# Kernel optimization log

Hardware: AMD Instinct MI355X
Metric: run time of the kernel (lower is better)

The kernel has to match this reference:

```python
import jax, jax.numpy as jnp
import numpy as np

E, D, A, F, K = 512, 1024, 128, 32, 31  # encoder_dim, decoder_dim, attention_dim, location_filters, kernel
B, T = 128, 512


def setup_inputs() -> dict:
    key = jax.random.key(0)
    ks = jax.random.split(key, 9)
    s = lambda *sh: 1.0 / np.sqrt(sh[-1])
    return {
        "encoder_outputs": jax.random.normal(ks[0], (B, T, E), jnp.float32),
        "decoder_state": jax.random.normal(ks[1], (B, D), jnp.float32),
        "prev_attention_weights": jax.random.uniform(ks[2], (B, T), jnp.float32),
        # parameters (torch Linear stores [out, in]; Conv1d [out, in, K])
        "W_enc": jax.random.normal(ks[3], (A, E), jnp.float32) * s(A, E),
        "W_dec": jax.random.normal(ks[4], (A, D), jnp.float32) * s(A, D),
        "conv_w": jax.random.normal(ks[5], (F, 1, K), jnp.float32) * (1.0 / np.sqrt(K)),
        "W_loc": jax.random.normal(ks[6], (A, F), jnp.float32) * s(A, F),
        "W_e": jax.random.normal(ks[7], (1, A), jnp.float32) * s(1, A),
        "b_e": jax.random.normal(ks[8], (1,), jnp.float32) * 0.01,
    }


def reference(encoder_outputs, decoder_state, prev_attention_weights,
              W_enc, W_dec, conv_w, W_loc, W_e, b_e):
    # encoder projection: [B,T,E] @ [E,A] -> [B,T,A]
    enc_p = jnp.einsum('bte,ae->bta', encoder_outputs, W_enc)
    # decoder projection: [B,D] -> [B,1,A]
    dec_p = jnp.einsum('bd,ad->ba', decoder_state, W_dec)[:, None, :]
    # location conv: [B,1,T] * [F,1,K] -> [B,F,T], 'same' padding
    loc = jax.lax.conv_general_dilated(
        prev_attention_weights[:, None, :], conv_w,
        window_strides=(1,), padding=[((K - 1) // 2, (K - 1) // 2)],
        dimension_numbers=('NCH', 'OIH', 'NCH'))
    # [B,F,T] -> [B,T,A]
    loc_p = jnp.einsum('bft,af->bta', loc, W_loc)
    # energies: [B,T]
    energies = jnp.einsum('bta,a->bt', jnp.tanh(enc_p + dec_p + loc_p), W_e[0]) + b_e[0]
    attention_weights = jax.nn.softmax(energies, axis=1)
    # context: [B,T] x [B,T,E] -> [B,E]
    context_vector = jnp.einsum('bt,bte->be', attention_weights, encoder_outputs)
    return context_vector, attention_weights
```

## Files before the change

### kernel.cpp

```cpp
#include <hip/hip_runtime.h>
#include <hip/hip_bf16.h>
#include <math.h>

namespace {
constexpr int EDIM  = 512;
constexpr int DDIM  = 1024;
constexpr int ADIM  = 128;
constexpr int FDIM  = 32;
constexpr int KW    = 31;
constexpr int BATCH = 128;
constexpr int TDIM  = 512;

typedef __attribute__((ext_vector_type(8))) short short8;
typedef __attribute__((ext_vector_type(4))) float floatx4;

__device__ __forceinline__ float fast_tanh(float x) {
  x = fminf(9.0f, fmaxf(-9.0f, x));
  float e = __expf(2.0f * x);
  return (e - 1.0f) / (e + 1.0f);
}

__device__ __forceinline__ ushort2 pack_bf16(float x, float y) {
  union { __hip_bfloat162 h; ushort2 u; } cv;
  cv.h = __float22bfloat162_rn(make_float2(x, y));
  return cv.u;
}

__device__ __forceinline__ short8 pack8(floatx4 a, floatx4 b) {
  union { ushort2 u[4]; short8 v; } o;
  o.u[0] = pack_bf16(a[0], a[1]); o.u[1] = pack_bf16(a[2], a[3]);
  o.u[2] = pack_bf16(b[0], b[1]); o.u[3] = pack_bf16(b[2], b[3]);
  return o.v;
}

__global__ __launch_bounds__(256)
void dec_proj_kernel(const float* __restrict__ dec,
                     const float* __restrict__ Wdec,
                     float* __restrict__ dec_p) {
  int b = blockIdx.x, az = blockIdx.y;
  int tid = threadIdx.x;
  int al = tid >> 3, seg = tid & 7;
  int a = az * 32 + al;
  const float* dv = dec + (size_t)b * DDIM;
  const float* wv = Wdec + (size_t)a * DDIM;
  float s = 0.f;
  #pragma unroll 8
  for (int it = 0; it < 32; ++it) {
    int d = it * 32 + seg * 4;
    float4 d4 = *(const float4*)(dv + d);
    float4 w4 = *(const float4*)(wv + d);
    s += d4.x * w4.x + d4.y * w4.y + d4.z * w4.z + d4.w * w4.w;
  }
  s += __shfl_xor(s, 1, 64);
  s += __shfl_xor(s, 2, 64);
  s += __shfl_xor(s, 4, 64);
  if (seg == 0) dec_p[b * ADIM + a] = s;
}

__global__ __launch_bounds__(256)
void energies_kernel(const float* __restrict__ enc,
                     const float* __restrict__ Wenc,
                     const float* __restrict__ pa,
                     const float* __restrict__ convw,
                     const float* __restrict__ Wloc,
                     const float* __restrict__ We,
                     const float* __restrict__ be,
                     const float* __restrict__ dec_p,
                     float* __restrict__ energ) {
  __shared__ ushort WencS[16384];
  __shared__ ushort convS[2048];
  __shared__ float pa_s[96];
  __shared__ float cw_s[FDIM * 33];

  const int tid  = threadIdx.x;
  const int b    = blockIdx.y;
  const int t0b  = blockIdx.x * 64;
  const int wave = tid >> 6, lane = tid & 63;
  const int lc = lane & 15, lq = lane >> 4;
  const int sw = lc & 7;

  if (tid < 94) {
    int gt = t0b - 15 + tid;
    pa_s[tid] = (gt >= 0 && gt < TDIM) ? pa[b * TDIM + gt] : 0.f;
  }
  for (int id = tid; id < FDIM * KW; id += 256)
    cw_s[(id / KW) * 33 + (id % KW)] = convw[id];
  __syncthreads();

  {
    const int tl = tid >> 2, fg = tid & 3;
    float cv[8];
    #pragma unroll
    for (int n = 0; n < 8; ++n) {
      int f = fg * 8 + n;
      float s = 0.f;
      #pragma unroll
      for (int k = 0; k < KW; ++k) s += pa_s[tl + k] * cw_s[f * 33 + k];
      cv[n] = s;
    }
    *(short8*)&convS[tl * 32 + fg * 8] =
        pack8((floatx4){cv[0], cv[1], cv[2], cv[3]},
              (floatx4){cv[4], cv[5], cv[6], cv[7]});
  }

  #pragma unroll
  for (int r = 0; r < 8; ++r) {
    int idx = tid + r * 256;
    int sup = idx >> 10, i2 = idx & 1023;
    int row = i2 >> 3, gc = (i2 & 7) ^ (row & 7);
    const float* g = Wenc + (size_t)row * EDIM + sup * 64 + gc * 8;
    *(short8*)&WencS[sup * 8192 + i2 * 8] =
        pack8(*(const floatx4*)g, *(const floatx4*)(g + 4));
  }

  const float* pA = enc + ((size_t)(b * TDIM + t0b + wave * 16 + lc)) * EDIM + lq * 8;
  floatx4 ca = *(const floatx4*)pA, cb = *(const floatx4*)(pA + 4);

  float dpv[8], wev[8];
  #pragma unroll
  for (int aT = 0; aT < 8; ++aT) {
    int a = aT * 16 + lc;
    dpv[aT] = dec_p[b * ADIM + a];
    wev[aT] = We[a];
  }

  floatx4 acc[8];
  #pragma unroll
  for (int aT = 0; aT < 8; ++aT) acc[aT] = (floatx4){0.f, 0.f, 0.f, 0.f};

  __syncthreads();

  for (int ph = 0; ph < 4; ++ph) {
    if (ph) {
      __syncthreads();
      #pragma unroll
      for (int r = 0; r < 8; ++r) {
        int idx = tid + r * 256;
        int sup = idx >> 10, i2 = idx & 1023;
        int row = i2 >> 3, gc = (i2 & 7) ^ (row & 7);
        const float* g = Wenc + (size_t)row * EDIM + ph * 128 + sup * 64 + gc * 8;
        *(short8*)&WencS[sup * 8192 + i2 * 8] =
            pack8(*(const floatx4*)g, *(const floatx4*)(g + 4));
      }
      __syncthreads();
    }
    #pragma unroll
    for (int st = 0; st < 4; ++st) {
      const int step = ph * 4 + st;
      floatx4 na = {0,0,0,0}, nb = {0,0,0,0};
      if (step < 15) {
        const float* q = pA + (step + 1) * 32;
        na = *(const floatx4*)q; nb = *(const floatx4*)(q + 4);
      }
      short8 af = pack8(ca, cb);
      const int cco = (((st & 1) * 4 + lq) ^ sw) * 8;
      const ushort* Bb = &WencS[(st >> 1) * 8192 + cco];
      #pragma unroll
      for (int aT = 0; aT < 8; ++aT) {
        short8 bf = *(const short8*)&Bb[(aT * 16 + lc) * 64];
        acc[aT] = __builtin_amdgcn_mfma_f32_16x16x32_bf16(af, bf, acc[aT], 0, 0, 0);
      }
      ca = na; cb = nb;
    }
  }

  {
    short8 afl = *(const short8*)&convS[(wave * 16 + lc) * 32 + lq * 8];
    #pragma unroll
    for (int aT = 0; aT < 8; ++aT) {
      const float* g = Wloc + (size_t)(aT * 16 + lc) * FDIM + lq * 8;
      short8 bfl = pack8(*(const floatx4*)g, *(const floatx4*)(g + 4));
      acc[aT] = __builtin_amdgcn_mfma_f32_16x16x32_bf16(afl, bfl, acc[aT], 0, 0, 0);
    }
  }

  const float be0 = be[0];
  {
    float es[4] = {0.f, 0.f, 0.f, 0.f};
    #pragma unroll
    for (int aT = 0; aT < 8; ++aT)
      #pragma unroll
      for (int i = 0; i < 4; ++i)
        es[i] += fast_tanh(acc[aT][i] + dpv[aT]) * wev[aT];
    #pragma unroll
    for (int m = 1; m < 16; m <<= 1)
      #pragma unroll
      for (int i = 0; i < 4; ++i) es[i] += __shfl_xor(es[i], m, 64);
    if (lc == 0) {
      floatx4 ev = {es[0] + be0, es[1] + be0, es[2] + be0, es[3] + be0};
      *(floatx4*)&energ[(size_t)b * TDIM + t0b + wave * 16 + lq * 4] = ev;
    }
  }
}

__global__ __launch_bounds__(256)
void softmax_context_kernel(const float* __restrict__ enc,
                            const float* __restrict__ energ,
                            float* __restrict__ attn,
                            float* __restrict__ ctx) {
  __shared__ float aw[TDIM];
  __shared__ float redm[4];
  __shared__ float reds[4];
  __shared__ float red2[128];
  const int b = blockIdx.y, ex = blockIdx.x, tid = threadIdx.x;
  const float* row = energ + (size_t)b * TDIM;
  float x0 = row[tid], x1 = row[tid + 256];
  float m = fmaxf(x0, x1);
  #pragma unroll
  for (int off = 32; off; off >>= 1) m = fmaxf(m, __shfl_xor(m, off, 64));
  int wid = tid >> 6, lane = tid & 63;
  if (lane == 0) redm[wid] = m;
  __syncthreads();
  m = fmaxf(fmaxf(redm[0], redm[1]), fmaxf(redm[2], redm[3]));
  float e0 = __expf(x0 - m), e1 = __expf(x1 - m);
  float s = e0 + e1;
  #pragma unroll
  for (int off = 32; off; off >>= 1) s += __shfl_xor(s, off, 64);
  if (lane == 0) reds[wid] = s;
  __syncthreads();
  s = reds[0] + reds[1] + reds[2] + reds[3];
  float inv = 1.0f / s;
  float w0 = e0 * inv, w1 = e1 * inv;
  aw[tid] = w0; aw[tid + 256] = w1;
  if (ex == 0) {
    attn[(size_t)b * TDIM + tid] = w0;
    attn[(size_t)b * TDIM + tid + 256] = w1;
  }
  __syncthreads();
  const int j = tid & 127, h = tid >> 7;
  const float* ep = enc + ((size_t)(b * TDIM + h * 256)) * EDIM + ex * 128 + j;
  float acc = 0.f;
  #pragma unroll 16
  for (int t = 0; t < 256; ++t) acc += aw[h * 256 + t] * ep[(size_t)t * EDIM];
  if (h == 1) red2[j] = acc;
  __syncthreads();
  if (h == 0) ctx[(size_t)b * EDIM + ex * 128 + j] = acc + red2[j];
}

__global__ __launch_bounds__(256)
void softmax_context_inplace_kernel(const float* __restrict__ enc,
                                    float* __restrict__ attn,
                                    float* __restrict__ ctx) {
  __shared__ float aw[TDIM];
  __shared__ float redm[4];
  __shared__ float reds[4];
  const int b = blockIdx.y, tid = threadIdx.x;
  float* row = attn + (size_t)b * TDIM;
  float x0 = row[tid], x1 = row[tid + 256];
  float m = fmaxf(x0, x1);
  #pragma unroll
  for (int off = 32; off; off >>= 1) m = fmaxf(m, __shfl_xor(m, off, 64));
  int wid = tid >> 6, lane = tid & 63;
  if (lane == 0) redm[wid] = m;
  __syncthreads();
  m = fmaxf(fmaxf(redm[0], redm[1]), fmaxf(redm[2], redm[3]));
  float e0 = __expf(x0 - m), e1 = __expf(x1 - m);
  float s = e0 + e1;
  #pragma unroll
  for (int off = 32; off; off >>= 1) s += __shfl_xor(s, off, 64);
  if (lane == 0) reds[wid] = s;
  __syncthreads();
  s = reds[0] + reds[1] + reds[2] + reds[3];
  float inv = 1.0f / s;
  float w0 = e0 * inv, w1 = e1 * inv;
  row[tid] = w0; row[tid + 256] = w1;
  aw[tid] = w0; aw[tid + 256] = w1;
  __syncthreads();
  const float* ep = enc + ((size_t)b * TDIM) * EDIM;
  float a0 = 0.f, a1 = 0.f;
  #pragma unroll 8
  for (int t = 0; t < TDIM; ++t) {
    float w = aw[t];
    a0 += w * ep[(size_t)t * EDIM + tid];
    a1 += w * ep[(size_t)t * EDIM + tid + 256];
  }
  ctx[(size_t)b * EDIM + tid] = a0;
  ctx[(size_t)b * EDIM + tid + 256] = a1;
}

}

extern "C" void kernel_launch(void* const* d_in, const int* in_sizes, int n_in,
                              void* d_out, int out_size, void* d_ws, size_t ws_size,
                              hipStream_t stream) {
  const float* enc   = (const float*)d_in[0];
  const float* dec   = (const float*)d_in[1];
  const float* pa    = (const float*)d_in[2];
  const float* Wenc  = (const float*)d_in[3];
  const float* Wdec  = (const float*)d_in[4];
  const float* convw = (const float*)d_in[5];
  const float* Wloc  = (const float*)d_in[6];
  const float* We    = (const float*)d_in[7];
  const float* be    = (const float*)d_in[8];

  float* ctx  = (float*)d_out;
  float* attn = (float*)d_out + BATCH * EDIM;

  float* dec_p = (float*)d_ws;
  float* energ = dec_p + BATCH * ADIM;

  const size_t need = (size_t)(BATCH * ADIM + BATCH * TDIM) * sizeof(float);

  dim3 g1(BATCH, 4);
  dec_proj_kernel<<<g1, 256, 0, stream>>>(dec, Wdec, dec_p);

  dim3 g2(TDIM / 64, BATCH);
  if (ws_size >= need) {
    energies_kernel<<<g2, 256, 0, stream>>>(enc, Wenc, pa, convw, Wloc, We, be,
                                            dec_p, energ);
    dim3 g3(4, BATCH);
    softmax_context_kernel<<<g3, 256, 0, stream>>>(enc, energ, attn, ctx);
  } else {
    energies_kernel<<<g2, 256, 0, stream>>>(enc, Wenc, pa, convw, Wloc, We, be,
                                            dec_p, attn);
    dim3 g3(1, BATCH);
    softmax_context_inplace_kernel<<<g3, 256, 0, stream>>>(enc, attn, ctx);
  }
}
```

Before: 279.9 us.

## Warp-specialize energies kernel with producer waves and LDS double buffering

Restructures the energies kernel into 768-thread blocks that each cover 128 time steps. Four producer waves stream encoder tiles and W_enc tiles into double-buffered LDS as bf16. Eight consumer waves run the MFMAs and synchronize with the producers through LDS atomic counters instead of block-wide barriers. The aim is to overlap global loads with matrix math and to halve the redundant W_enc reloads per block, at the cost of spin-wait overhead, larger LDS use and lower occupancy.

```diff
diff --git a/kernel.cpp b/kernel.cpp
--- a/kernel.cpp
+++ b/kernel.cpp
@@ -11,6 +11,9 @@
 constexpr int BATCH = 128;
 constexpr int TDIM  = 512;
 
+constexpr int LSTR = 40;
+constexpr int TILE = 128 * LSTR;
+
 typedef __attribute__((ext_vector_type(8))) short short8;
 typedef __attribute__((ext_vector_type(4))) float floatx4;
 
@@ -31,6 +34,13 @@
   o.u[0] = pack_bf16(a[0], a[1]); o.u[1] = pack_bf16(a[2], a[3]);
   o.u[2] = pack_bf16(b[0], b[1]); o.u[3] = pack_bf16(b[2], b[3]);
   return o.v;
+}
+
+__device__ __forceinline__ int ld_acq(int* p) {
+  return __hip_atomic_load(p, __ATOMIC_ACQUIRE, __HIP_MEMORY_SCOPE_WORKGROUP);
+}
+__device__ __forceinline__ void add_rel(int* p) {
+  __hip_atomic_fetch_add(p, 1, __ATOMIC_RELEASE, __HIP_MEMORY_SCOPE_WORKGROUP);
 }
 
 __global__ __launch_bounds__(256)
@@ -57,7 +67,7 @@
   if (seg == 0) dec_p[b * ADIM + a] = s;
 }
 
-__global__ __launch_bounds__(256)
+__global__ __launch_bounds__(768)
 void energies_kernel(const float* __restrict__ enc,
                      const float* __restrict__ Wenc,
                      const float* __restrict__ pa,
@@ -67,25 +77,64 @@
                      const float* __restrict__ be,
                      const float* __restrict__ dec_p,
                      float* __restrict__ energ) {
-  __shared__ ushort WencS[16384];
-  __shared__ ushort convS[2048];
-  __shared__ float pa_s[96];
+  __shared__ ushort tiles[2 * 2 * TILE];
+  __shared__ ushort convS[4096];
+  __shared__ float pa_s[160];
   __shared__ float cw_s[FDIM * 33];
+  __shared__ int ready_a[2], ready_b[2], done_c[2], conv_done;
 
   const int tid  = threadIdx.x;
   const int b    = blockIdx.y;
-  const int t0b  = blockIdx.x * 64;
+  const int t0b  = blockIdx.x * 128;
   const int wave = tid >> 6, lane = tid & 63;
+
+  if (tid == 0) {
+    ready_a[0] = ready_a[1] = ready_b[0] = ready_b[1] = 0;
+    done_c[0] = done_c[1] = 0;
+    conv_done = 0;
+  }
+  if (tid >= 512 && tid < 512 + 158) {
+    int gt = t0b - 15 + (tid - 512);
+    pa_s[tid - 512] = (gt >= 0 && gt < TDIM) ? pa[b * TDIM + gt] : 0.f;
+  }
+  if (tid < 512)
+    for (int id = tid; id < FDIM * KW; id += 512)
+      cw_s[(id / KW) * 33 + (id % KW)] = convw[id];
+  __syncthreads();
+
+  if (wave >= 8) {
+    const bool isA = (wave < 10);
+    const int p = wave & 1;
+    const float* gbase = isA ? enc + ((size_t)(b * TDIM + t0b)) * EDIM : Wenc;
+    ushort* lbase = tiles + (isA ? 0 : TILE);
+    int* myready = isA ? ready_a : ready_b;
+    for (int kt = 0; kt < 16; ++kt) {
+      const int s = kt & 1, i = kt >> 1;
+      if (kt >= 2)
+        while (ld_acq(&done_c[s]) < 8 * i) __builtin_amdgcn_s_sleep(2);
+      ushort* slot = lbase + s * 2 * TILE;
+      floatx4 v[8];
+      #pragma unroll
+      for (int j = 0; j < 4; ++j) {
+        int idx = j * 64 + lane;
+        int row = p * 64 + (idx >> 2), c = idx & 3;
+        const float* g = gbase + (size_t)row * EDIM + kt * 32 + c * 8;
+        v[2 * j]     = *(const floatx4*)g;
+        v[2 * j + 1] = *(const floatx4*)(g + 4);
+      }
+      #pragma unroll
+      for (int j = 0; j < 4; ++j) {
+        int idx = j * 64 + lane;
+        int row = p * 64 + (idx >> 2), c = idx & 3;
+        *(short8*)&slot[row * LSTR + c * 8] = pack8(v[2 * j], v[2 * j + 1]);
+      }
+      __threadfence_block();
+      if (lane == 0) add_rel(&myready[s]);
+    }
+    return;
+  }
+
   const int lc = lane & 15, lq = lane >> 4;
-  const int sw = lc & 7;
-
-  if (tid < 94) {
-    int gt = t0b - 15 + tid;
-    pa_s[tid] = (gt >= 0 && gt < TDIM) ? pa[b * TDIM + gt] : 0.f;
-  }
-  for (int id = tid; id < FDIM * KW; id += 256)
-    cw_s[(id / KW) * 33 + (id % KW)] = convw[id];
-  __syncthreads();
 
   {
     const int tl = tid >> 2, fg = tid & 3;
@@ -102,20 +151,41 @@
         pack8((floatx4){cv[0], cv[1], cv[2], cv[3]},
               (floatx4){cv[4], cv[5], cv[6], cv[7]});
   }
-
-  #pragma unroll
-  for (int r = 0; r < 8; ++r) {
-    int idx = tid + r * 256;
-    int sup = idx >> 10, i2 = idx & 1023;
-    int row = i2 >> 3, gc = (i2 & 7) ^ (row & 7);
-    const float* g = Wenc + (size_t)row * EDIM + sup * 64 + gc * 8;
-    *(short8*)&WencS[sup * 8192 + i2 * 8] =
-        pack8(*(const floatx4*)g, *(const floatx4*)(g + 4));
-  }
-
-  const float* pA = enc + ((size_t)(b * TDIM + t0b + wave * 16 + lc)) * EDIM + lq * 8;
-  floatx4 ca = *(const floatx4*)pA, cb = *(const floatx4*)(pA + 4);
-
+  __threadfence_block();
+  if (lane == 0) add_rel(&conv_done);
+
+  floatx4 acc[8];
+  #pragma unroll
+  for (int aT = 0; aT < 8; ++aT) acc[aT] = (floatx4){0.f, 0.f, 0.f, 0.f};
+
+  for (int kt = 0; kt < 16; ++kt) {
+    const int s = kt & 1, i = kt >> 1;
+    const int need = 2 * (i + 1);
+    while (ld_acq(&ready_a[s]) < need || ld_acq(&ready_b[s]) < need)
+      __builtin_amdgcn_s_sleep(2);
+    const ushort* As_ = tiles + s * 2 * TILE;
+    const ushort* Bs_ = As_ + TILE;
+    short8 af = *(const short8*)&As_[(wave * 16 + lc) * LSTR + lq * 8];
+    #pragma unroll
+    for (int aT = 0; aT < 8; ++aT) {
+      short8 bf = *(const short8*)&Bs_[(aT * 16 + lc) * LSTR + lq * 8];
+      acc[aT] = __builtin_amdgcn_mfma_f32_16x16x32_bf16(af, bf, acc[aT], 0, 0, 0);
+    }
+    if (lane == 0) add_rel(&done_c[s]);
+  }
+
+  while (ld_acq(&conv_done) < 8) __builtin_amdgcn_s_sleep(2);
+  {
+    short8 afl = *(const short8*)&convS[(wave * 16 + lc) * 32 + lq * 8];
+    #pragma unroll
+    for (int aT = 0; aT < 8; ++aT) {
+      const float* g = Wloc + (size_t)(aT * 16 + lc) * FDIM + lq * 8;
+      short8 bfl = pack8(*(const floatx4*)g, *(const floatx4*)(g + 4));
+      acc[aT] = __builtin_amdgcn_mfma_f32_16x16x32_bf16(afl, bfl, acc[aT], 0, 0, 0);
+    }
+  }
+
+  const float be0 = be[0];
   float dpv[8], wev[8];
   #pragma unroll
   for (int aT = 0; aT < 8; ++aT) {
@@ -123,58 +193,6 @@
     dpv[aT] = dec_p[b * ADIM + a];
     wev[aT] = We[a];
   }
-
-  floatx4 acc[8];
-  #pragma unroll
-  for (int aT = 0; aT < 8; ++aT) acc[aT] = (floatx4){0.f, 0.f, 0.f, 0.f};
-
-  __syncthreads();
-
-  for (int ph = 0; ph < 4; ++ph) {
-    if (ph) {
-      __syncthreads();
-      #pragma unroll
-      for (int r = 0; r < 8; ++r) {
-        int idx = tid + r * 256;
-        int sup = idx >> 10, i2 = idx & 1023;
-        int row = i2 >> 3, gc = (i2 & 7) ^ (row & 7);
-        const float* g = Wenc + (size_t)row * EDIM + ph * 128 + sup * 64 + gc * 8;
-        *(short8*)&WencS[sup * 8192 + i2 * 8] =
-            pack8(*(const floatx4*)g, *(const floatx4*)(g + 4));
-      }
-      __syncthreads();
-    }
-    #pragma unroll
-    for (int st = 0; st < 4; ++st) {
-      const int step = ph * 4 + st;
-      floatx4 na = {0,0,0,0}, nb = {0,0,0,0};
-      if (step < 15) {
-        const float* q = pA + (step + 1) * 32;
-        na = *(const floatx4*)q; nb = *(const floatx4*)(q + 4);
-      }
-      short8 af = pack8(ca, cb);
-      const int cco = (((st & 1) * 4 + lq) ^ sw) * 8;
-      const ushort* Bb = &WencS[(st >> 1) * 8192 + cco];
-      #pragma unroll
-      for (int aT = 0; aT < 8; ++aT) {
-        short8 bf = *(const short8*)&Bb[(aT * 16 + lc) * 64];
-        acc[aT] = __builtin_amdgcn_mfma_f32_16x16x32_bf16(af, bf, acc[aT], 0, 0, 0);
-      }
-      ca = na; cb = nb;
-    }
-  }
-
-  {
-    short8 afl = *(const short8*)&convS[(wave * 16 + lc) * 32 + lq * 8];
-    #pragma unroll
-    for (int aT = 0; aT < 8; ++aT) {
-      const float* g = Wloc + (size_t)(aT * 16 + lc) * FDIM + lq * 8;
-      short8 bfl = pack8(*(const floatx4*)g, *(const floatx4*)(g + 4));
-      acc[aT] = __builtin_amdgcn_mfma_f32_16x16x32_bf16(afl, bfl, acc[aT], 0, 0, 0);
-    }
-  }
-
-  const float be0 = be[0];
   {
     float es[4] = {0.f, 0.f, 0.f, 0.f};
     #pragma unroll
@@ -304,14 +322,14 @@
   dim3 g1(BATCH, 4);
   dec_proj_kernel<<<g1, 256, 0, stream>>>(dec, Wdec, dec_p);
 
-  dim3 g2(TDIM / 64, BATCH);
+  dim3 g2(TDIM / 128, BATCH);
   if (ws_size >= need) {
-    energies_kernel<<<g2, 256, 0, stream>>>(enc, Wenc, pa, convw, Wloc, We, be,
+    energies_kernel<<<g2, 768, 0, stream>>>(enc, Wenc, pa, convw, Wloc, We, be,
                                             dec_p, energ);
     dim3 g3(4, BATCH);
     softmax_context_kernel<<<g3, 256, 0, stream>>>(enc, energ, attn, ctx);
   } else {
-    energies_kernel<<<g2, 256, 0, stream>>>(enc, Wenc, pa, convw, Wloc, We, be,
+    energies_kernel<<<g2, 768, 0, stream>>>(enc, Wenc, pa, convw, Wloc, We, be,
                                             dec_p, attn);
     dim3 g3(1, BATCH);
     softmax_context_inplace_kernel<<<g3, 256, 0, stream>>>(enc, attn, ctx);
```

New measurement: 245.9 us. 1.14x faster.
